# Kernel tuning notes

Measured on AMD Instinct MI355X. Metric: run time of the kernel, lower is better.

Reference implementation:

```python
import jax, jax.numpy as jnp
import numpy as np

HK, DK, HV, DV = 16, 128, 32, 128
VE = (HV // HK) * DV  # 256
CHUNK = 64
KSZ = 4
EPS = 1e-12


def l2_normalize(x):
    sq = jnp.sum(x * x, axis=-1, keepdims=True)
    return x * jax.lax.rsqrt(sq + EPS)


def causal_dwconv_silu(x_bct, w, b):
    # x_bct: [B, C, T]; w: [C, 1, K]; b: [C]; causal depthwise conv then SiLU
    C = x_bct.shape[1]
    y = jax.lax.conv_general_dilated(
        x_bct, w, window_strides=(1,), padding=[(KSZ - 1, 0)],
        dimension_numbers=('NCH', 'OIH', 'NCH'), feature_group_count=C)
    return jax.nn.silu(y + b[None, :, None])


def setup_inputs() -> dict:
    key = jax.random.key(0)
    ks = jax.random.split(key, 12)
    B, T, H = 2, 2048, 2048
    s = 0.02
    return {
        'x': jax.random.normal(ks[0], (B, T, H), jnp.float32),
        'state': jnp.zeros((B, HK, DK, VE), jnp.float32),
        'Wq': jax.random.normal(ks[1], (HK * DK, H), jnp.float32) * s,
        'Wk': jax.random.normal(ks[2], (HK * DK, H), jnp.float32) * s,
        'Wv': jax.random.normal(ks[3], (HV * DV, H), jnp.float32) * s,
        'Wo': jax.random.normal(ks[4], (H, HV * DV), jnp.float32) * s,
        'Wa': jax.random.normal(ks[5], (HK, H), jnp.float32) * s,
        'Wb': jax.random.normal(ks[6], (HK, H), jnp.float32) * s,
        'qcW': jax.random.normal(ks[7], (HK * DK, 1, KSZ), jnp.float32) * 0.3,
        'qcB': jnp.zeros((HK * DK,), jnp.float32),
        'kcW': jax.random.normal(ks[8], (HK * DK, 1, KSZ), jnp.float32) * 0.3,
        'kcB': jnp.zeros((HK * DK,), jnp.float32),
        'vcW': jax.random.normal(ks[9], (HV * DV, 1, KSZ), jnp.float32) * 0.3,
        'vcB': jnp.zeros((HV * DV,), jnp.float32),
    }


def _forward(x, state, Wq, Wk, Wv, Wo, Wa, Wb, qcW, qcB, kcW, kcB, vcW, vcB):
    B, T, H = x.shape
    Cn = CHUNK
    # T is a multiple of CHUNK here (no padding needed)
    nc = T // Cn
    x_bct = jnp.transpose(x, (0, 2, 1))  # [B, H, T]
    # 1x1-conv projections == channelwise linear
    q = causal_dwconv_silu(jnp.einsum('qh,bht->bqt', Wq, x_bct), qcW, qcB)
    k = causal_dwconv_silu(jnp.einsum('qh,bht->bqt', Wk, x_bct), kcW, kcB)
    v = causal_dwconv_silu(jnp.einsum('vh,bht->bvt', Wv, x_bct), vcW, vcB)
    alpha = jax.nn.sigmoid(jnp.einsum('gh,bht->bgt', Wa, x_bct))  # [B,HK,T]
    beta = jax.nn.sigmoid(jnp.einsum('gh,bht->bgt', Wb, x_bct))

    q = jnp.transpose(q, (0, 2, 1)).reshape(B, T, HK, DK)
    k = jnp.transpose(k, (0, 2, 1)).reshape(B, T, HK, DK)
    # regroup value heads by key head: [B,T,HV,DV] -> [B,T,HK,VE]
    v = jnp.transpose(v, (0, 2, 1)).reshape(B, T, HK, VE)
    alpha = jnp.transpose(alpha, (0, 2, 1))  # [B,T,HK]
    beta = jnp.transpose(beta, (0, 2, 1))

    q = l2_normalize(q)
    k = l2_normalize(k)

    # time-major, chunked: [nc, Cn, B, HK, ...]
    def tmchunk(a):
        a = jnp.moveaxis(a, 1, 0)  # [T, B, ...]
        return a.reshape((nc, Cn) + a.shape[1:])

    qc, kc, vc, ac, bc = map(tmchunk, (q, k, v, alpha, beta))

    def step(s, inp):
        qt, kt, vt, at, bt = inp  # qt/kt [B,HK,DK], vt [B,HK,VE], at/bt [B,HK]
        s = s * at[..., None, None]
        retrieved = jnp.einsum('bhkv,bhk->bhv', s, kt)
        err = vt - retrieved
        s = s + bt[..., None, None] * (kt[..., :, None] * err[..., None, :])
        ot = jnp.einsum('bhkv,bhk->bhv', s, qt)
        return s, ot

    @jax.checkpoint
    def chunk_step(s, ch):
        return jax.lax.scan(step, s, ch)

    state, outs = jax.lax.scan(chunk_step, state, (qc, kc, vc, ac, bc))
    # outs: [nc, Cn, B, HK, VE] -> [B, T, HV*DV]
    out = outs.reshape(T, B, HK * VE)
    out = jnp.moveaxis(out, 0, 1)
    out = jnp.einsum('btv,ov->bto', out, Wo)
    return out, state


def reference(x, state, Wq, Wk, Wv, Wo, Wa, Wb, qcW, qcB, kcW, kcB, vcW, vcB):
    return _forward(x, state, Wq, Wk, Wv, Wo, Wa, Wb, qcW, qcB, kcW, kcB, vcW, vcB)
```

## Files before the change

kernel.cpp:

```cpp
#include <hip/hip_runtime.h>
#include <hip/hip_bf16.h>

typedef __attribute__((ext_vector_type(8))) __bf16 bf16x8;
typedef __attribute__((ext_vector_type(8))) short short8;
typedef __attribute__((ext_vector_type(4))) float floatx4;
using u16 = unsigned short;

#define GLOBAL_AS __attribute__((address_space(1)))
#define LDS_AS    __attribute__((address_space(3)))

__device__ __forceinline__ float b2f(u16 u) {
    union { unsigned int i; float f; } v; v.i = ((unsigned int)u) << 16; return v.f;
}
__device__ __forceinline__ u16 f2b(float f) {
    __hip_bfloat16 h = __float2bfloat16(f);
    return __builtin_bit_cast(u16, h);
}
__device__ __forceinline__ float ldf(const void* p, long i, bool isf32) {
    return isf32 ? ((const float*)p)[i] : b2f(((const u16*)p)[i]);
}
__device__ __forceinline__ void gload_lds16(const void* g, void* l) {
    __builtin_amdgcn_global_load_lds((const GLOBAL_AS unsigned int*)g,
                                     (LDS_AS unsigned int*)l, 16, 0, 0);
}
__device__ __forceinline__ float red8(float x) {
    int xi, yi;
    xi = __builtin_bit_cast(int, x);
    yi = __builtin_amdgcn_update_dpp(xi, xi, 0xB1, 0xF, 0xF, false);
    x += __builtin_bit_cast(float, yi);
    xi = __builtin_bit_cast(int, x);
    yi = __builtin_amdgcn_update_dpp(xi, xi, 0x4E, 0xF, 0xF, false);
    x += __builtin_bit_cast(float, yi);
    xi = __builtin_bit_cast(int, x);
    yi = __builtin_amdgcn_update_dpp(xi, xi, 0x141, 0xF, 0xF, false);
    x += __builtin_bit_cast(float, yi);
    return x;
}
__device__ __forceinline__ void unpack2(int d, float& lo, float& hi) {
    lo = __builtin_bit_cast(float, (int)((unsigned)d << 16));
    hi = __builtin_bit_cast(float, d & 0xffff0000);
}
__device__ __forceinline__ void unpack8(int4 d, float* f) {
    unpack2(d.x, f[0], f[1]); unpack2(d.y, f[2], f[3]);
    unpack2(d.z, f[4], f[5]); unpack2(d.w, f[6], f[7]);
}

__global__ void detect_dtype(const unsigned int* __restrict__ x, int* __restrict__ flag) {
    const int lane = threadIdx.x;
    int sane = 0;
    for (int i = lane; i < 256; i += 64) {
        const unsigned e = (x[i] >> 23) & 0xFF;
        sane += (e >= 100 && e <= 140) ? 1 : 0;
    }
#pragma unroll
    for (int m = 1; m < 64; m <<= 1) sane += __shfl_xor(sane, m, 64);
    if (lane == 0) *flag = (sane >= 128) ? 1 : 0;
}

__global__ __launch_bounds__(256) void cvt_bf16(
    const void* __restrict__ in, u16* __restrict__ out, long n, const int* __restrict__ flag) {
    const bool f32 = (*flag != 0);
    const long i = ((long)blockIdx.x * 256 + threadIdx.x) * 8;
    if (i >= n) return;
    if (f32) {
        const float* p = (const float*)in + i;
        floatx4 a = *(const floatx4*)p, b = *(const floatx4*)(p + 4);
        short8 o;
        o[0] = (short)f2b(a[0]); o[1] = (short)f2b(a[1]);
        o[2] = (short)f2b(a[2]); o[3] = (short)f2b(a[3]);
        o[4] = (short)f2b(b[0]); o[5] = (short)f2b(b[1]);
        o[6] = (short)f2b(b[2]); o[7] = (short)f2b(b[3]);
        *(short8*)(out + i) = o;
    } else {
        *(int4*)(out + i) = *(const int4*)((const u16*)in + i);
    }
}

__global__ __launch_bounds__(256) void gemm_bt128(
    const u16* __restrict__ A, const u16* __restrict__ B, void* __restrict__ C,
    int M, int N, int K, int cmode, const int* __restrict__ flag) {
    const bool c32 = (cmode == 1) || (cmode == 2 && *flag != 0);
    __shared__ __align__(16) u16 As[128 * 32];
    __shared__ __align__(16) u16 Bs[128 * 32];
    const int tid = threadIdx.x, lane = tid & 63, wave = tid >> 6;
    const int bm = blockIdx.y * 128, bn = blockIdx.x * 128;
    const int wm = (wave >> 1) * 64, wn = (wave & 1) * 64;
    const int fr = lane & 15, fq = lane >> 4;
    floatx4 acc[4][4] = {};

    const int srow = tid >> 2, scol = (tid & 3) * 8;
    const long abase = (long)(bm + srow) * K + scol;
    const long bbase = (long)(bn + srow) * K + scol;
    char* lA = (char*)As + (tid & ~63) * 16;
    char* lB = (char*)Bs + (tid & ~63) * 16;

    for (int k0 = 0; k0 < K; k0 += 32) {
        __syncthreads();
        gload_lds16(A + abase + k0, lA);
        gload_lds16(A + abase + (long)64 * K + k0, lA + 4096);
        gload_lds16(B + bbase + k0, lB);
        gload_lds16(B + bbase + (long)64 * K + k0, lB + 4096);
        __syncthreads();
        bf16x8 af[4], bf[4];
#pragma unroll
        for (int i = 0; i < 4; i++) {
            af[i] = __builtin_bit_cast(bf16x8, *(const short8*)&As[(wm + i * 16 + fr) * 32 + fq * 8]);
            bf[i] = __builtin_bit_cast(bf16x8, *(const short8*)&Bs[(wn + i * 16 + fr) * 32 + fq * 8]);
        }
#pragma unroll
        for (int mi = 0; mi < 4; mi++)
#pragma unroll
            for (int ni = 0; ni < 4; ni++)
                acc[mi][ni] = __builtin_amdgcn_mfma_f32_16x16x32_bf16(
                    af[mi], bf[ni], acc[mi][ni], 0, 0, 0);
    }
#pragma unroll
    for (int mi = 0; mi < 4; mi++)
#pragma unroll
        for (int ni = 0; ni < 4; ni++)
#pragma unroll
            for (int r = 0; r < 4; r++) {
                const int m = bm + wm + mi * 16 + fq * 4 + r;
                const int n = bn + wn + ni * 16 + fr;
                const float val = acc[mi][ni][r];
                const long ci = (long)m * N + n;
                if (c32) ((float*)C)[ci] = val;
                else ((u16*)C)[ci] = f2b(val);
            }
}

__global__ __launch_bounds__(256) void ab_gemm(
    const u16* __restrict__ xb, const u16* __restrict__ wab,
    float* __restrict__ alphaT, float* __restrict__ betaT) {
    __shared__ __align__(16) u16 As[64 * 64];
    __shared__ __align__(16) u16 Bs[32 * 64];
    const int tid = threadIdx.x, lane = tid & 63, wave = tid >> 6;
    const int bm = blockIdx.x * 64;
    const int fr = lane & 15, fq = lane >> 4;
    floatx4 acc[2] = {};

    const int srow = tid >> 3, scol = (tid & 7) * 8;
    char* lA = (char*)As + (tid & ~63) * 16;
    char* lB = (char*)Bs + (tid & ~63) * 16;

    for (int k0 = 0; k0 < 2048; k0 += 64) {
        __syncthreads();
        gload_lds16(xb + (long)(bm + srow) * 2048 + k0 + scol, lA);
        gload_lds16(xb + (long)(bm + 32 + srow) * 2048 + k0 + scol, lA + 4096);
        gload_lds16(wab + (long)srow * 2048 + k0 + scol, lB);
        __syncthreads();
#pragma unroll
        for (int ks = 0; ks < 2; ks++) {
            bf16x8 af = __builtin_bit_cast(bf16x8,
                *(const short8*)&As[(wave * 16 + fr) * 64 + ks * 32 + fq * 8]);
#pragma unroll
            for (int nt = 0; nt < 2; nt++) {
                bf16x8 bf = __builtin_bit_cast(bf16x8,
                    *(const short8*)&Bs[(nt * 16 + fr) * 64 + ks * 32 + fq * 8]);
                acc[nt] = __builtin_amdgcn_mfma_f32_16x16x32_bf16(af, bf, acc[nt], 0, 0, 0);
            }
        }
    }
#pragma unroll
    for (int nt = 0; nt < 2; nt++)
#pragma unroll
        for (int r = 0; r < 4; r++) {
            const int m = bm + wave * 16 + fq * 4 + r;
            const int n = nt * 16 + fr;
            const int b = m >> 11, t = m & 2047;
            const float s = 1.f / (1.f + __expf(-acc[nt][r]));
            if (n < 16) alphaT[((long)b * 16 + n) * 2048 + t] = s;
            else betaT[((long)b * 16 + (n - 16)) * 2048 + t] = s;
        }
}

__global__ __launch_bounds__(256) void conv_silu_norm(
    const u16* __restrict__ pre, const void* __restrict__ cw,
    const void* __restrict__ cb, u16* __restrict__ out, const int* __restrict__ flag) {
    const bool f32 = (*flag != 0);
    const int bt = blockIdx.x;
    const int t = bt & 2047;
    const int tid = threadIdx.x;
    const int c0 = tid * 8;
    float y[8];
    float ss = 0.f;
#pragma unroll
    for (int j = 0; j < 8; j++) {
        const int c = c0 + j;
        float acc = ldf(cb, c, f32);
#pragma unroll
        for (int i = 0; i < 4; i++) {
            if (t - 3 + i >= 0)
                acc += ldf(cw, c * 4 + i, f32) * b2f(pre[(long)(bt - 3 + i) * 2048 + c]);
        }
        const float s = acc / (1.f + __expf(-acc));
        y[j] = s;
        ss += s * s;
    }
#pragma unroll
    for (int m = 1; m < 16; m <<= 1) ss += __shfl_xor(ss, m, 64);
    const float inv = rsqrtf(ss + 1e-12f);
#pragma unroll
    for (int j = 0; j < 8; j++) out[(long)bt * 2048 + c0 + j] = f2b(y[j] * inv);
}

__global__ __launch_bounds__(256) void conv_silu_v(
    const u16* __restrict__ pre, const void* __restrict__ cw,
    const void* __restrict__ cb, u16* __restrict__ out, const int* __restrict__ flag) {
    const bool f32 = (*flag != 0);
    const int bt = blockIdx.x;
    const int t = bt & 2047;
    const int tid = threadIdx.x;
    const int c0 = tid * 16;
#pragma unroll
    for (int j = 0; j < 16; j++) {
        const int c = c0 + j;
        float acc = ldf(cb, c, f32);
#pragma unroll
        for (int i = 0; i < 4; i++) {
            if (t - 3 + i >= 0)
                acc += ldf(cw, c * 4 + i, f32) * b2f(pre[(long)(bt - 3 + i) * 4096 + c]);
        }
        out[(long)bt * 4096 + c] = f2b(acc / (1.f + __expf(-acc)));
    }
}

__global__ __launch_bounds__(256) void recurrence_kernel(
    const u16* __restrict__ qn, const u16* __restrict__ kn,
    const u16* __restrict__ vn, const float* __restrict__ alphaT,
    const float* __restrict__ betaT, const void* __restrict__ state_in,
    u16* __restrict__ outs, void* __restrict__ d_out, const int* __restrict__ flag) {
    const bool f32 = (*flag != 0);
    const int blk = blockIdx.x;
    const int vb = blk & 7, h = (blk >> 3) & 15, b = blk >> 7;
    const int tid = threadIdx.x, lane = tid & 63, wave = tid >> 6;
    const int kg = lane & 7, vq = lane >> 3;
    const int vloc = wave * 8 + vq;
    const int vglob = vb * 32 + vloc;

    float S[16];
    const long stbase = ((long)(b * 16 + h) * 128 + kg * 16) * 256 + vglob;
#pragma unroll
    for (int j = 0; j < 16; j++) S[j] = ldf(state_in, stbase + (long)j * 256, f32);

    __shared__ __align__(16) float kf[2][16 * 128];
    __shared__ __align__(16) float qf[2][16 * 128];
    __shared__ __align__(16) float vf[2][16 * 32];

    const int srow = tid >> 4, sc8 = (tid & 15) * 8, vc2 = (tid & 15) * 2;
    const long gkq0 = ((long)b * 2048 + srow) * 2048 + h * 128 + sc8;
    const long gv0  = ((long)b * 2048 + srow) * 4096 + h * 256 + vb * 32 + vc2;
    const long abase = (long)(b * 16 + h) * 2048;

    int4 gk, gq;
    unsigned int gv;
    float ga, gb;

    auto stage_write = [&](int buf) {
        const int kgg = sc8 >> 4, i0 = (sc8 >> 2) & 3;
        float fk[8], fq_[8];
        unpack8(gk, fk);
        unpack8(gq, fq_);
        const int base = srow * 128 + kgg * 4;
        *(floatx4*)&kf[buf][base + i0 * 32]       = floatx4{fk[0], fk[1], fk[2], fk[3]};
        *(floatx4*)&kf[buf][base + (i0 + 1) * 32] = floatx4{fk[4], fk[5], fk[6], fk[7]};
        *(floatx4*)&qf[buf][base + i0 * 32]       = floatx4{fq_[0], fq_[1], fq_[2], fq_[3]};
        *(floatx4*)&qf[buf][base + (i0 + 1) * 32] = floatx4{fq_[4], fq_[5], fq_[6], fq_[7]};
        vf[buf][srow * 32 + vc2]     = b2f((u16)(gv & 0xffffu));
        vf[buf][srow * 32 + vc2 + 1] = b2f((u16)(gv >> 16));
    };

    gk = *(const int4*)(kn + gkq0);
    gq = *(const int4*)(qn + gkq0);
    gv = *(const unsigned int*)(vn + gv0);
    ga = alphaT[abase + (lane & 15)];
    gb = betaT[abase + (lane & 15)];
    stage_write(0);
    __syncthreads();

    for (int c = 0; c < 128; ++c) {
        const int cur = c & 1;
        const float aw = ga, bw = gb;
        if (c + 1 < 128) {
            const long off = (long)(c + 1) * 16 * 2048;
            gk = *(const int4*)(kn + gkq0 + off);
            gq = *(const int4*)(qn + gkq0 + off);
            gv = *(const unsigned int*)(vn + gv0 + (long)(c + 1) * 16 * 4096);
            ga = alphaT[abase + (c + 1) * 16 + (lane & 15)];
            gb = betaT[abase + (c + 1) * 16 + (lane & 15)];
        }

        const float* kfp = kf[cur];
        const float* qfp = qf[cur];
        const float* vfp = vf[cur];

        floatx4 ka[4], qa[4];
#pragma unroll
        for (int i = 0; i < 4; i++) {
            ka[i] = *(const floatx4*)&kfp[i * 32 + kg * 4];
            qa[i] = *(const floatx4*)&qfp[i * 32 + kg * 4];
        }
        float vcur = vfp[vloc];

#pragma unroll
        for (int tt = 0; tt < 16; ++tt) {
            floatx4 ka_n[4], qa_n[4];
            float v_n = 0.f;
            if (tt < 15) {
#pragma unroll
                for (int i = 0; i < 4; i++) {
                    ka_n[i] = *(const floatx4*)&kfp[(tt + 1) * 128 + i * 32 + kg * 4];
                    qa_n[i] = *(const floatx4*)&qfp[(tt + 1) * 128 + i * 32 + kg * 4];
                }
                v_n = vfp[(tt + 1) * 32 + vloc];
            }
            const float a = __builtin_bit_cast(float,
                __builtin_amdgcn_readlane(__builtin_bit_cast(int, aw), tt));
            const float bb = __builtin_bit_cast(float,
                __builtin_amdgcn_readlane(__builtin_bit_cast(int, bw), tt));
            float r0 = 0.f, r1 = 0.f;
#pragma unroll
            for (int i = 0; i < 4; i++)
#pragma unroll
                for (int j = 0; j < 4; j++) {
                    const int idx = i * 4 + j;
                    if (idx < 8) r0 = fmaf(S[idx], ka[i][j], r0);
                    else         r1 = fmaf(S[idx], ka[i][j], r1);
                }
            const float r = red8(r0 + r1);
            const float err = fmaf(-a, r, vcur);
            const float cc = bb * err;
            float o0 = 0.f, o1 = 0.f;
#pragma unroll
            for (int i = 0; i < 4; i++)
#pragma unroll
                for (int j = 0; j < 4; j++) {
                    const int idx = i * 4 + j;
                    S[idx] = fmaf(cc, ka[i][j], a * S[idx]);
                    if (idx < 8) o0 = fmaf(S[idx], qa[i][j], o0);
                    else         o1 = fmaf(S[idx], qa[i][j], o1);
                }
            const float o = red8(o0 + o1);
            if (kg == 0)
                outs[((long)b * 2048 + c * 16 + tt) * 4096 + h * 256 + vglob] = f2b(o);
            if (tt < 15) {
#pragma unroll
                for (int i = 0; i < 4; i++) { ka[i] = ka_n[i]; qa[i] = qa_n[i]; }
                vcur = v_n;
            }
        }

        if (c + 1 < 128) stage_write(cur ^ 1);
        __syncthreads();
    }

#pragma unroll
    for (int j = 0; j < 16; j++) {
        const long idx = 8388608L + stbase + (long)j * 256;
        if (f32) ((float*)d_out)[idx] = S[j];
        else ((u16*)d_out)[idx] = f2b(S[j]);
    }
}

extern "C" void kernel_launch(void* const* d_in, const int* in_sizes, int n_in,
                              void* d_out, int out_size, void* d_ws, size_t ws_size,
                              hipStream_t stream) {
    const void* x   = d_in[0];
    const void* st0 = d_in[1];
    const void* Wq  = d_in[2];
    const void* Wk  = d_in[3];
    const void* Wv  = d_in[4];
    const void* Wo  = d_in[5];
    const void* Wa  = d_in[6];
    const void* Wb  = d_in[7];
    const void* qcW = d_in[8];
    const void* qcB = d_in[9];
    const void* kcW = d_in[10];
    const void* kcB = d_in[11];
    const void* vcW = d_in[12];
    const void* vcB = d_in[13];

    const int M = 4096;
    const long MB = 1024L * 1024L;
    char* w = (char*)d_ws;
    int*   flag   = (int*)w;
    float* alphaT = (float*)(w + 1024);
    float* betaT  = (float*)(w + 1024 + 262144);
    u16*   wab    = (u16*)(w + 1024 + 524288);
    u16* xb    = (u16*)(w + 1 * MB);
    u16* wqb   = (u16*)(w + 17 * MB);
    u16* wkb   = (u16*)(w + 25 * MB);
    u16* wvb   = (u16*)(w + 33 * MB);
    u16* qpreb = (u16*)(w + 49 * MB);
    u16* kpreb = (u16*)(w + 65 * MB);
    u16* vpreb = (u16*)(w + 81 * MB);
    u16* qn    = (u16*)(w + 113 * MB);
    u16* kn    = (u16*)(w + 129 * MB);
    u16* vn    = (u16*)(w + 145 * MB);
    u16* wob   = xb;
    u16* outs  = qpreb;

    dim3 blk(256);
    detect_dtype<<<dim3(1), dim3(64), 0, stream>>>((const unsigned int*)x, flag);

    cvt_bf16<<<dim3(4096), blk, 0, stream>>>(x,  xb,  8388608L, flag);
    cvt_bf16<<<dim3(2048), blk, 0, stream>>>(Wq, wqb, 4194304L, flag);
    cvt_bf16<<<dim3(2048), blk, 0, stream>>>(Wk, wkb, 4194304L, flag);
    cvt_bf16<<<dim3(4096), blk, 0, stream>>>(Wv, wvb, 8388608L, flag);
    cvt_bf16<<<dim3(16),   blk, 0, stream>>>(Wa, wab, 32768L, flag);
    cvt_bf16<<<dim3(16),   blk, 0, stream>>>(Wb, wab + 32768, 32768L, flag);

    gemm_bt128<<<dim3(2048 / 128, M / 128), blk, 0, stream>>>(xb, wqb, qpreb, M, 2048, 2048, 3, flag);
    gemm_bt128<<<dim3(2048 / 128, M / 128), blk, 0, stream>>>(xb, wkb, kpreb, M, 2048, 2048, 3, flag);
    gemm_bt128<<<dim3(4096 / 128, M / 128), blk, 0, stream>>>(xb, wvb, vpreb, M, 4096, 2048, 3, flag);
    ab_gemm<<<dim3(64), blk, 0, stream>>>(xb, wab, alphaT, betaT);

    cvt_bf16<<<dim3(4096), blk, 0, stream>>>(Wo, wob, 8388608L, flag);

    conv_silu_norm<<<dim3(M), blk, 0, stream>>>(qpreb, qcW, qcB, qn, flag);
    conv_silu_norm<<<dim3(M), blk, 0, stream>>>(kpreb, kcW, kcB, kn, flag);
    conv_silu_v<<<dim3(M), blk, 0, stream>>>(vpreb, vcW, vcB, vn, flag);

    recurrence_kernel<<<dim3(256), blk, 0, stream>>>(qn, kn, vn, alphaT, betaT, st0,
                                                     outs, d_out, flag);

    gemm_bt128<<<dim3(2048 / 128, M / 128), blk, 0, stream>>>(outs, wob, d_out, M, 2048, 4096, 2, flag);
}
```

Measured before the change: 1.706 ms.

## Split recurrence across 512 blocks with 16-lane k reduction and 8-row state

Reworks the recurrence kernel so each block covers 16 value columns instead of 32, doubling the grid to 512 blocks. Each lane now holds 8 state rows instead of 16, and the dot-product reduction runs over 16 lanes with an extra DPP step. The LDS layout, the v staging (only half the threads load v) and the per-step k/q prefetch are simplified to match. The aim is to shorten the latency-bound serial per-step chain and fill more CUs, at the cost of redundant k/q staging per block and one extra reduction step per dot product.

```diff
diff --git a/kernel.cpp b/kernel.cpp
--- a/kernel.cpp
+++ b/kernel.cpp
@@ -23,7 +23,7 @@
     __builtin_amdgcn_global_load_lds((const GLOBAL_AS unsigned int*)g,
                                      (LDS_AS unsigned int*)l, 16, 0, 0);
 }
-__device__ __forceinline__ float red8(float x) {
+__device__ __forceinline__ float red16(float x) {
     int xi, yi;
     xi = __builtin_bit_cast(int, x);
     yi = __builtin_amdgcn_update_dpp(xi, xi, 0xB1, 0xF, 0xF, false);
@@ -33,6 +33,9 @@
     x += __builtin_bit_cast(float, yi);
     xi = __builtin_bit_cast(int, x);
     yi = __builtin_amdgcn_update_dpp(xi, xi, 0x141, 0xF, 0xF, false);
+    x += __builtin_bit_cast(float, yi);
+    xi = __builtin_bit_cast(int, x);
+    yi = __builtin_amdgcn_update_dpp(xi, xi, 0x140, 0xF, 0xF, false);
     x += __builtin_bit_cast(float, yi);
     return x;
 }
@@ -232,49 +235,51 @@
     u16* __restrict__ outs, void* __restrict__ d_out, const int* __restrict__ flag) {
     const bool f32 = (*flag != 0);
     const int blk = blockIdx.x;
-    const int vb = blk & 7, h = (blk >> 3) & 15, b = blk >> 7;
+    const int vb = blk & 15, h = (blk >> 4) & 15, b = blk >> 8;
     const int tid = threadIdx.x, lane = tid & 63, wave = tid >> 6;
-    const int kg = lane & 7, vq = lane >> 3;
-    const int vloc = wave * 8 + vq;
-    const int vglob = vb * 32 + vloc;
-
-    float S[16];
-    const long stbase = ((long)(b * 16 + h) * 128 + kg * 16) * 256 + vglob;
-#pragma unroll
-    for (int j = 0; j < 16; j++) S[j] = ldf(state_in, stbase + (long)j * 256, f32);
+    const int kg = lane & 15, vq = lane >> 4;
+    const int vloc = wave * 4 + vq;
+    const int vglob = vb * 16 + vloc;
+
+    float S[8];
+    const long stbase = ((long)(b * 16 + h) * 128 + kg * 8) * 256 + vglob;
+#pragma unroll
+    for (int j = 0; j < 8; j++) S[j] = ldf(state_in, stbase + (long)j * 256, f32);
 
     __shared__ __align__(16) float kf[2][16 * 128];
     __shared__ __align__(16) float qf[2][16 * 128];
-    __shared__ __align__(16) float vf[2][16 * 32];
-
-    const int srow = tid >> 4, sc8 = (tid & 15) * 8, vc2 = (tid & 15) * 2;
-    const long gkq0 = ((long)b * 2048 + srow) * 2048 + h * 128 + sc8;
-    const long gv0  = ((long)b * 2048 + srow) * 4096 + h * 256 + vb * 32 + vc2;
+    __shared__ __align__(16) float vf[2][16 * 16];
+
+    const int srow = tid >> 4, skg = tid & 15;
+    const long gkq0 = ((long)b * 2048 + srow) * 2048 + h * 128 + skg * 8;
+    const int vrow = tid >> 3, vc2 = (tid & 7) * 2;
+    const long gv0 = ((long)b * 2048 + vrow) * 4096 + h * 256 + vb * 16 + vc2;
     const long abase = (long)(b * 16 + h) * 2048;
 
     int4 gk, gq;
-    unsigned int gv;
+    unsigned int gv = 0;
     float ga, gb;
 
     auto stage_write = [&](int buf) {
-        const int kgg = sc8 >> 4, i0 = (sc8 >> 2) & 3;
         float fk[8], fq_[8];
         unpack8(gk, fk);
         unpack8(gq, fq_);
-        const int base = srow * 128 + kgg * 4;
-        *(floatx4*)&kf[buf][base + i0 * 32]       = floatx4{fk[0], fk[1], fk[2], fk[3]};
-        *(floatx4*)&kf[buf][base + (i0 + 1) * 32] = floatx4{fk[4], fk[5], fk[6], fk[7]};
-        *(floatx4*)&qf[buf][base + i0 * 32]       = floatx4{fq_[0], fq_[1], fq_[2], fq_[3]};
-        *(floatx4*)&qf[buf][base + (i0 + 1) * 32] = floatx4{fq_[4], fq_[5], fq_[6], fq_[7]};
-        vf[buf][srow * 32 + vc2]     = b2f((u16)(gv & 0xffffu));
-        vf[buf][srow * 32 + vc2 + 1] = b2f((u16)(gv >> 16));
+        const int base = srow * 128 + skg * 4;
+        *(floatx4*)&kf[buf][base]      = floatx4{fk[0], fk[1], fk[2], fk[3]};
+        *(floatx4*)&kf[buf][base + 64] = floatx4{fk[4], fk[5], fk[6], fk[7]};
+        *(floatx4*)&qf[buf][base]      = floatx4{fq_[0], fq_[1], fq_[2], fq_[3]};
+        *(floatx4*)&qf[buf][base + 64] = floatx4{fq_[4], fq_[5], fq_[6], fq_[7]};
+        if (tid < 128) {
+            vf[buf][vrow * 16 + vc2]     = b2f((u16)(gv & 0xffffu));
+            vf[buf][vrow * 16 + vc2 + 1] = b2f((u16)(gv >> 16));
+        }
     };
 
     gk = *(const int4*)(kn + gkq0);
     gq = *(const int4*)(qn + gkq0);
-    gv = *(const unsigned int*)(vn + gv0);
-    ga = alphaT[abase + (lane & 15)];
-    gb = betaT[abase + (lane & 15)];
+    if (tid < 128) gv = *(const unsigned int*)(vn + gv0);
+    ga = alphaT[abase + kg];
+    gb = betaT[abase + kg];
     stage_write(0);
     __syncthreads();
 
@@ -285,69 +290,47 @@
             const long off = (long)(c + 1) * 16 * 2048;
             gk = *(const int4*)(kn + gkq0 + off);
             gq = *(const int4*)(qn + gkq0 + off);
-            gv = *(const unsigned int*)(vn + gv0 + (long)(c + 1) * 16 * 4096);
-            ga = alphaT[abase + (c + 1) * 16 + (lane & 15)];
-            gb = betaT[abase + (c + 1) * 16 + (lane & 15)];
+            if (tid < 128) gv = *(const unsigned int*)(vn + gv0 + (long)(c + 1) * 16 * 4096);
+            ga = alphaT[abase + (c + 1) * 16 + kg];
+            gb = betaT[abase + (c + 1) * 16 + kg];
         }
 
         const float* kfp = kf[cur];
         const float* qfp = qf[cur];
         const float* vfp = vf[cur];
-
-        floatx4 ka[4], qa[4];
-#pragma unroll
-        for (int i = 0; i < 4; i++) {
-            ka[i] = *(const floatx4*)&kfp[i * 32 + kg * 4];
-            qa[i] = *(const floatx4*)&qfp[i * 32 + kg * 4];
-        }
-        float vcur = vfp[vloc];
+        const long obase = ((long)b * 2048 + c * 16) * 4096 + h * 256 + vglob;
 
 #pragma unroll
         for (int tt = 0; tt < 16; ++tt) {
-            floatx4 ka_n[4], qa_n[4];
-            float v_n = 0.f;
-            if (tt < 15) {
-#pragma unroll
-                for (int i = 0; i < 4; i++) {
-                    ka_n[i] = *(const floatx4*)&kfp[(tt + 1) * 128 + i * 32 + kg * 4];
-                    qa_n[i] = *(const floatx4*)&qfp[(tt + 1) * 128 + i * 32 + kg * 4];
-                }
-                v_n = vfp[(tt + 1) * 32 + vloc];
-            }
+            const floatx4 ka0 = *(const floatx4*)&kfp[tt * 128 + kg * 4];
+            const floatx4 ka1 = *(const floatx4*)&kfp[tt * 128 + kg * 4 + 64];
+            const floatx4 qa0 = *(const floatx4*)&qfp[tt * 128 + kg * 4];
+            const floatx4 qa1 = *(const floatx4*)&qfp[tt * 128 + kg * 4 + 64];
+            const float vcur = vfp[tt * 16 + vloc];
             const float a = __builtin_bit_cast(float,
                 __builtin_amdgcn_readlane(__builtin_bit_cast(int, aw), tt));
             const float bb = __builtin_bit_cast(float,
                 __builtin_amdgcn_readlane(__builtin_bit_cast(int, bw), tt));
             float r0 = 0.f, r1 = 0.f;
 #pragma unroll
-            for (int i = 0; i < 4; i++)
-#pragma unroll
-                for (int j = 0; j < 4; j++) {
-                    const int idx = i * 4 + j;
-                    if (idx < 8) r0 = fmaf(S[idx], ka[i][j], r0);
-                    else         r1 = fmaf(S[idx], ka[i][j], r1);
-                }
-            const float r = red8(r0 + r1);
+            for (int j = 0; j < 4; j++) {
+                r0 = fmaf(S[j], ka0[j], r0);
+                r1 = fmaf(S[4 + j], ka1[j], r1);
+            }
+            const float r = red16(r0 + r1);
             const float err = fmaf(-a, r, vcur);
             const float cc = bb * err;
             float o0 = 0.f, o1 = 0.f;
 #pragma unroll
-            for (int i = 0; i < 4; i++)
-#pragma unroll
-                for (int j = 0; j < 4; j++) {
-                    const int idx = i * 4 + j;
-                    S[idx] = fmaf(cc, ka[i][j], a * S[idx]);
-                    if (idx < 8) o0 = fmaf(S[idx], qa[i][j], o0);
-                    else         o1 = fmaf(S[idx], qa[i][j], o1);
-                }
-            const float o = red8(o0 + o1);
+            for (int j = 0; j < 4; j++) {
+                S[j] = fmaf(cc, ka0[j], a * S[j]);
+                S[4 + j] = fmaf(cc, ka1[j], a * S[4 + j]);
+                o0 = fmaf(S[j], qa0[j], o0);
+                o1 = fmaf(S[4 + j], qa1[j], o1);
+            }
+            const float o = red16(o0 + o1);
             if (kg == 0)
-                outs[((long)b * 2048 + c * 16 + tt) * 4096 + h * 256 + vglob] = f2b(o);
-            if (tt < 15) {
-#pragma unroll
-                for (int i = 0; i < 4; i++) { ka[i] = ka_n[i]; qa[i] = qa_n[i]; }
-                vcur = v_n;
-            }
+                outs[obase + (long)tt * 4096] = f2b(o);
         }
 
         if (c + 1 < 128) stage_write(cur ^ 1);
@@ -355,7 +338,7 @@
     }
 
 #pragma unroll
-    for (int j = 0; j < 16; j++) {
+    for (int j = 0; j < 8; j++) {
         const long idx = 8388608L + stbase + (long)j * 256;
         if (f32) ((float*)d_out)[idx] = S[j];
         else ((u16*)d_out)[idx] = f2b(S[j]);
@@ -421,7 +404,7 @@
     conv_silu_norm<<<dim3(M), blk, 0, stream>>>(kpreb, kcW, kcB, kn, flag);
     conv_silu_v<<<dim3(M), blk, 0, stream>>>(vpreb, vcW, vcB, vn, flag);
 
-    recurrence_kernel<<<dim3(256), blk, 0, stream>>>(qn, kn, vn, alphaT, betaT, st0,
+    recurrence_kernel<<<dim3(512), blk, 0, stream>>>(qn, kn, vn, alphaT, betaT, st0,
                                                      outs, d_out, flag);
 
     gemm_bt128<<<dim3(2048 / 128, M / 128), blk, 0, stream>>>(outs, wob, d_out, M, 2048, 4096, 2, flag);
```

Result: slower. 1.805 ms (+5.8%).
